# Kernel tuning notes

Hardware: AMD Instinct MI355X
Metric: run time of the kernel (lower is better)

The kernel has to match this reference:

```python
import jax, jax.numpy as jnp
import numpy as np

EPS = 1e-6

def hardswish(x):
    return x * jnp.clip(x + 3.0, 0.0, 6.0) * (1.0 / 6.0)

def setup_inputs() -> dict:
    key = jax.random.key(0)
    ks = jax.random.split(key, 12)
    B, C, T, V, K, O = 64, 64, 512, 25, 3, 64
    x = jax.random.normal(ks[0], (B, C, T, V), jnp.float32)
    A_fixed = jax.random.uniform(ks[1], (K, V, V), jnp.float32)          # fixed structural partitions (buffer)
    A_learned = jax.random.normal(ks[2], (K, V, V), jnp.float32) * 0.01  # learned adjacency (init ~0)
    W_gcn = jax.random.normal(ks[3], (K, O, C), jnp.float32) * (1.0 / np.sqrt(C))  # 1x1 convs, no bias
    gcn_scale = jax.random.uniform(ks[4], (O,), jnp.float32, 0.5, 1.5)   # folded eval-mode BN
    gcn_bias = jax.random.normal(ks[5], (O,), jnp.float32) * 0.05
    tcn_dw = jax.random.normal(ks[6], (O, 1, 9, 1), jnp.float32) * 0.1   # depthwise temporal conv k=9
    tcn_pw = jax.random.normal(ks[7], (O, O), jnp.float32) * (1.0 / np.sqrt(O))  # pointwise conv
    tcn_scale1 = jax.random.uniform(ks[8], (O,), jnp.float32, 0.5, 1.5)
    tcn_bias1 = jax.random.normal(ks[9], (O,), jnp.float32) * 0.05
    tcn_scale2 = jax.random.uniform(ks[10], (O,), jnp.float32, 0.5, 1.5)
    tcn_bias2 = jax.random.normal(ks[11], (O,), jnp.float32) * 0.05
    return {"x": x, "A_fixed": A_fixed, "A_learned": A_learned, "W_gcn": W_gcn,
            "gcn_scale": gcn_scale, "gcn_bias": gcn_bias, "tcn_dw": tcn_dw, "tcn_pw": tcn_pw,
            "tcn_scale1": tcn_scale1, "tcn_bias1": tcn_bias1, "tcn_scale2": tcn_scale2, "tcn_bias2": tcn_bias2}

def _bn(x, scale, bias):
    # eval-mode BatchNorm2d folded to per-channel affine, channel axis=1
    return x * scale[None, :, None, None] + bias[None, :, None, None]

def reference(x, A_fixed, A_learned, W_gcn, gcn_scale, gcn_bias,
              tcn_dw, tcn_pw, tcn_scale1, tcn_bias1, tcn_scale2, tcn_bias2):
    res = x
    K = A_fixed.shape[0]
    # --- EfficientGCN-exact K-way learned-adjacency normalization ---
    A = jnp.abs(A_fixed + A_learned)                       # (K,V,V)
    d = jax.lax.rsqrt(jnp.clip(jnp.sum(A, axis=2), EPS, None))  # torch sum(dim=1) -> row sums, D^{-1/2}
    A_norm = d[:, :, None] * A * d[:, None, :]             # (K,V,V)
    # --- fused adjacency matmul + 1x1 conv accumulate over K ---
    # x:(B,C,T,V) @ A_norm:(K,V,W) then channel mix W_gcn:(K,O,C), averaged over K
    y = jnp.einsum('bctv,kvw,koc->botw', x, A_norm, W_gcn) / K
    y = hardswish(_bn(y, gcn_scale, gcn_bias))
    # --- DepthwiseSepTCN: depthwise temporal conv(k=9,pad=4) -> BN -> hswish -> pointwise -> BN ---
    t = jax.lax.conv_general_dilated(y, tcn_dw, (1, 1), ((4, 4), (0, 0)),
                                     dimension_numbers=('NCHW', 'OIHW', 'NCHW'),
                                     feature_group_count=y.shape[1])
    t = hardswish(_bn(t, tcn_scale1, tcn_bias1))
    t = jnp.einsum('bctv,oc->botv', t, tcn_pw)
    t = _bn(t, tcn_scale2, tcn_bias2)
    # residual is Identity (in_ch==out_ch, stride==1); DropPath rate 0 -> identity
    return hardswish(t + res)
```

## Files before the change

### kernel.cpp

```cpp
#include <hip/hip_runtime.h>
#include <math.h>

typedef unsigned short ushort_t;
typedef __attribute__((ext_vector_type(8))) short short8;
typedef __attribute__((ext_vector_type(4))) short short4v;
typedef __attribute__((ext_vector_type(4))) float f32x4;

#define B_ 64
#define C_ 64
#define T_ 512
#define V_ 25
#define K_ 3
#define O_ 64

__device__ __forceinline__ float hswish(float v) {
    return v * fminf(fmaxf(v + 3.0f, 0.0f), 6.0f) * (1.0f / 6.0f);
}
__device__ __forceinline__ ushort_t f2bf(float f) {
    unsigned u = __float_as_uint(f);
    unsigned r = (u + 0x7FFFu + ((u >> 16) & 1u)) >> 16;
    return (ushort_t)r;
}
__device__ __forceinline__ float bf2f(ushort_t h) {
    return __uint_as_float(((unsigned)h) << 16);
}

__global__ void k0_prep(const float* __restrict__ Af, const float* __restrict__ Al,
                        const float* __restrict__ Wg, const float* __restrict__ pw,
                        ushort_t* __restrict__ An2T, ushort_t* __restrict__ W2,
                        ushort_t* __restrict__ pw2) {
    __shared__ float Aabs[K_ * V_ * V_];
    __shared__ float dsh[K_ * V_];
    int tid = threadIdx.x;
    for (int i = tid; i < K_ * V_ * V_; i += 256) Aabs[i] = fabsf(Af[i] + Al[i]);
    __syncthreads();
    for (int r = tid; r < K_ * V_; r += 256) {
        float s = 0.0f;
        for (int j = 0; j < V_; j++) s += Aabs[r * V_ + j];
        dsh[r] = rsqrtf(fmaxf(s, 1e-6f));
    }
    __syncthreads();
    for (int i = tid; i < 80 * 32; i += 256) {
        int kw = i >> 5, v = i & 31;
        float val = 0.0f;
        if (kw < 75 && v < 25) {
            int k = (kw >= 50) ? 2 : (kw >= 25 ? 1 : 0);
            int w = kw - k * 25;
            val = dsh[k * 25 + v] * Aabs[(k * 25 + v) * 25 + w] * dsh[k * 25 + w];
        }
        An2T[i] = f2bf(val);
    }
    for (int i = tid; i < 64 * 192; i += 256) {
        int o = i / 192, kc = i % 192;
        int k = kc >> 6, c = kc & 63;
        W2[i] = f2bf(Wg[(k * 64 + o) * 64 + c] * (1.0f / 3.0f));
    }
    for (int i = tid; i < 64 * 64; i += 256) pw2[i] = f2bf(pw[i]);
}

__global__ __launch_bounds__(256) void k1_gcn(
    const float* __restrict__ x, const ushort_t* __restrict__ An2T,
    const ushort_t* __restrict__ W2, const float* __restrict__ gs,
    const float* __restrict__ gb, ushort_t* __restrict__ y) {
    __shared__ ushort_t xa2[100 * 200];
    float* xs = (float*)xa2;

    int bid = blockIdx.x;
    int b = bid >> 7;
    int t0 = (bid & 127) * 4;
    int tid = threadIdx.x;
    int wave = tid >> 6, lane = tid & 63;
    int m16 = lane & 15, g = lane >> 4;

#pragma unroll
    for (int i = 0; i < 7; i++) {
        int li = tid + 256 * i;
        if (li < 1600) {
            int c = li / 25, f4 = li % 25;
            const float* src = x + ((size_t)(b * 64 + c) * 512 + t0) * 25 + f4 * 4;
            *(f32x4*)(xs + c * 100 + f4 * 4) = *(const f32x4*)src;
        }
    }

    short8 bfA[5];
#pragma unroll
    for (int n = 0; n < 5; n++)
        bfA[n] = *(const short8*)(An2T + (n * 16 + m16) * 32 + g * 8);

    __syncthreads();

    int v0 = g * 8;
    short8 af[4];
#pragma unroll
    for (int mt = 0; mt < 4; mt++) {
        int ct = (wave * 4 + mt) * 16 + m16;
#pragma unroll
        for (int j = 0; j < 8; j++) {
            int v = v0 + j;
            float f = (v < 25) ? xs[25 * ct + v] : 0.0f;
            af[mt][j] = (short)f2bf(f);
        }
    }
    __syncthreads();

#pragma unroll
    for (int mt = 0; mt < 4; mt++) {
        int Mt = wave * 4 + mt;
        f32x4 acc[5];
#pragma unroll
        for (int n = 0; n < 5; n++) {
            acc[n] = (f32x4){0.f, 0.f, 0.f, 0.f};
            acc[n] = __builtin_amdgcn_mfma_f32_16x16x32_bf16(af[mt], bfA[n], acc[n], 0, 0, 0);
        }
        int cc = Mt * 4 + g;
#pragma unroll
        for (int n = 0; n < 5; n++) {
            int kw = n * 16 + m16;
            if (kw < 75) {
                int k = (kw >= 50) ? 2 : (kw >= 25 ? 1 : 0);
                int w = kw - k * 25;
#pragma unroll
                for (int r = 0; r < 4; r++)
                    xa2[(r * 25 + w) * 200 + k * 64 + cc] = f2bf(acc[n][r]);
            }
        }
    }
    __syncthreads();

    short8 afW[6];
#pragma unroll
    for (int kt = 0; kt < 6; kt++)
        afW[kt] = *(const short8*)(W2 + (wave * 16 + m16) * 192 + kt * 32 + g * 8);
    f32x4 gs4 = *(const f32x4*)(gs + wave * 16 + g * 4);
    f32x4 gb4 = *(const f32x4*)(gb + wave * 16 + g * 4);
    for (int nt = 0; nt < 7; nt++) {
        int tw = nt * 16 + m16;
        int twr = (tw < 100) ? tw : 99;
        f32x4 acc = (f32x4){0.f, 0.f, 0.f, 0.f};
#pragma unroll
        for (int kt = 0; kt < 6; kt++) {
            short8 bf = *(const short8*)(xa2 + twr * 200 + kt * 32 + g * 8);
            acc = __builtin_amdgcn_mfma_f32_16x16x32_bf16(afW[kt], bf, acc, 0, 0, 0);
        }
        if (tw < 100) {
            short4v pack;
#pragma unroll
            for (int r = 0; r < 4; r++) {
                float z = acc[r] * gs4[r] + gb4[r];
                pack[r] = (short)f2bf(hswish(z));
            }
            *(short4v*)(y + ((size_t)b * 12800 + t0 * 25 + tw) * 64 + wave * 16 + g * 4) = pack;
        }
    }
}

__global__ __launch_bounds__(256, 3) void k2_tcn(
    const ushort_t* __restrict__ y, const float* __restrict__ x,
    const float* __restrict__ dw, const ushort_t* __restrict__ pw2,
    const float* __restrict__ s1v, const float* __restrict__ b1v,
    const float* __restrict__ s2v, const float* __restrict__ b2v,
    float* __restrict__ out) {
    __shared__ f32x4 smemv[3264];
    ushort_t* ys = (ushort_t*)smemv;
    float* fb = (float*)smemv;

    int bid = blockIdx.x;
    int b = bid >> 6;
    int t0 = (bid & 63) * 8;
    int tid = threadIdx.x;
    int wave = tid >> 6, lane = tid & 63;
    int m16 = lane & 15, g = lane >> 4;

    const ushort_t* yb = y + (size_t)b * 12800 * 64;
    int tvbase = t0 * 25 - 100;
#pragma unroll
    for (int i = 0; i < 13; i++) {
        int li = tid + 256 * i;
        if (li < 3200) {
            int row = li >> 3;
            int col = (li & 7) * 8;
            int tvg = tvbase + row;
            short8 val = (short8){0, 0, 0, 0, 0, 0, 0, 0};
            if (tvg >= 0 && tvg < 12800)
                val = *(const short8*)(yb + (size_t)tvg * 64 + col);
            *(short8*)(ys + row * 64 + col) = val;
        }
    }
    __syncthreads();

    int cg = tid & 15, c0 = cg * 4;
    float dwc[4][9], s1r[4], b1r[4];
#pragma unroll
    for (int cj = 0; cj < 4; cj++) {
#pragma unroll
        for (int dt = 0; dt < 9; dt++) dwc[cj][dt] = dw[(c0 + cj) * 9 + dt];
        s1r[cj] = s1v[c0 + cj];
        b1r[cj] = b1v[c0 + cj];
    }
    short4v thv[13];
#pragma unroll
    for (int i = 0; i < 13; i++) {
        int tv = (tid >> 4) + 16 * i;
        float a0 = 0, a1 = 0, a2 = 0, a3 = 0;
        if (tv < 200) {
#pragma unroll
            for (int dt = 0; dt < 9; dt++) {
                short4v yv = *(const short4v*)(ys + (tv + dt * 25) * 64 + c0);
                a0 += dwc[0][dt] * bf2f((ushort_t)yv[0]);
                a1 += dwc[1][dt] * bf2f((ushort_t)yv[1]);
                a2 += dwc[2][dt] * bf2f((ushort_t)yv[2]);
                a3 += dwc[3][dt] * bf2f((ushort_t)yv[3]);
            }
        }
        short4v p;
        p[0] = (short)f2bf(hswish(a0 * s1r[0] + b1r[0]));
        p[1] = (short)f2bf(hswish(a1 * s1r[1] + b1r[1]));
        p[2] = (short)f2bf(hswish(a2 * s1r[2] + b1r[2]));
        p[3] = (short)f2bf(hswish(a3 * s1r[3] + b1r[3]));
        thv[i] = p;
    }
    __syncthreads();

#pragma unroll
    for (int i = 0; i < 13; i++) {
        int tv = (tid >> 4) + 16 * i;
        if (tv < 200) *(short4v*)(ys + tv * 64 + c0) = thv[i];
    }
    __syncthreads();

    short8 afP[2];
#pragma unroll
    for (int kt = 0; kt < 2; kt++)
        afP[kt] = *(const short8*)(pw2 + (wave * 16 + m16) * 64 + kt * 32 + g * 8);
    f32x4 s2_4 = *(const f32x4*)(s2v + wave * 16 + g * 4);
    f32x4 b2_4 = *(const f32x4*)(b2v + wave * 16 + g * 4);
    f32x4 accs[13];
#pragma unroll
    for (int nt = 0; nt < 13; nt++) {
        int tw = nt * 16 + m16;
        int twc = (tw < 200) ? tw : 199;
        f32x4 acc = (f32x4){0.f, 0.f, 0.f, 0.f};
#pragma unroll
        for (int kt = 0; kt < 2; kt++) {
            short8 bf = *(const short8*)(ys + twc * 64 + kt * 32 + g * 8);
            acc = __builtin_amdgcn_mfma_f32_16x16x32_bf16(afP[kt], bf, acc, 0, 0, 0);
        }
        accs[nt] = acc;
    }
    __syncthreads();

#pragma unroll
    for (int nt = 0; nt < 13; nt++) {
        int tw = nt * 16 + m16;
        if (tw < 200) {
#pragma unroll
            for (int r = 0; r < 4; r++)
                fb[(wave * 16 + g * 4 + r) * 204 + tw] = accs[nt][r] * s2_4[r] + b2_4[r];
        }
    }
    __syncthreads();

#pragma unroll
    for (int i = 0; i < 13; i++) {
        int l = tid + 256 * i;
        if (l < 3200) {
            int o = l / 50, c4 = l % 50;
            f32x4 v = *(const f32x4*)(fb + o * 204 + c4 * 4);
            size_t gi = (size_t)(b * 64 + o) * 12800 + t0 * 25 + c4 * 4;
            f32x4 xr = *(const f32x4*)(x + gi);
            f32x4 res;
#pragma unroll
            for (int r = 0; r < 4; r++) res[r] = hswish(v[r] + xr[r]);
            *(f32x4*)(out + gi) = res;
        }
    }
}

extern "C" void kernel_launch(void* const* d_in, const int* in_sizes, int n_in,
                              void* d_out, int out_size, void* d_ws, size_t ws_size,
                              hipStream_t stream) {
    const float* x   = (const float*)d_in[0];
    const float* Af  = (const float*)d_in[1];
    const float* Al  = (const float*)d_in[2];
    const float* Wg  = (const float*)d_in[3];
    const float* gs  = (const float*)d_in[4];
    const float* gb  = (const float*)d_in[5];
    const float* dw  = (const float*)d_in[6];
    const float* pw  = (const float*)d_in[7];
    const float* s1v = (const float*)d_in[8];
    const float* b1v = (const float*)d_in[9];
    const float* s2v = (const float*)d_in[10];
    const float* b2v = (const float*)d_in[11];
    float* out = (float*)d_out;

    ushort_t* An2T = (ushort_t*)d_ws;
    ushort_t* W2   = An2T + 2560;
    ushort_t* pw2  = W2 + 12288;
    ushort_t* ybf  = (ushort_t*)((char*)d_ws + 65536);

    k0_prep<<<1, 256, 0, stream>>>(Af, Al, Wg, pw, An2T, W2, pw2);
    k1_gcn<<<B_ * (T_ / 4), 256, 0, stream>>>(x, An2T, W2, gs, gb, ybf);
    k2_tcn<<<B_ * (T_ / 8), 256, 0, stream>>>(ybf, x, dw, pw2, s1v, b1v, s2v, b2v, out);
}
```

Before: 708.5 us.

## Use direct global-to-LDS loads and write TCN output straight from MFMA accumulators

In both kernels the input staging into shared memory now uses global_load_lds 16-byte transfers, so data goes straight into LDS instead of through registers. The k2 interior tiles take this path, while the two boundary time tiles keep the zero-padded register copy. The k2 epilogue no longer stages results through a shared-memory transpose. Each lane fuses BN2, the residual add and hardswish and writes scalar floats directly from the accumulators. This removes two barriers and an LDS round trip, at the cost of narrower, less coalesced residual reads and output stores.

```diff
diff --git a/kernel.cpp b/kernel.cpp
--- a/kernel.cpp
+++ b/kernel.cpp
@@ -78,7 +78,10 @@
         if (li < 1600) {
             int c = li / 25, f4 = li % 25;
             const float* src = x + ((size_t)(b * 64 + c) * 512 + t0) * 25 + f4 * 4;
-            *(f32x4*)(xs + c * 100 + f4 * 4) = *(const f32x4*)src;
+            __builtin_amdgcn_global_load_lds(
+                (const __attribute__((address_space(1))) unsigned*)src,
+                (__attribute__((address_space(3))) unsigned*)(xs + li * 4),
+                16, 0, 0);
         }
     }
 
@@ -160,9 +163,7 @@
     const float* __restrict__ s1v, const float* __restrict__ b1v,
     const float* __restrict__ s2v, const float* __restrict__ b2v,
     float* __restrict__ out) {
-    __shared__ f32x4 smemv[3264];
-    ushort_t* ys = (ushort_t*)smemv;
-    float* fb = (float*)smemv;
+    __shared__ ushort_t ys[400 * 64];
 
     int bid = blockIdx.x;
     int b = bid >> 6;
@@ -173,17 +174,31 @@
 
     const ushort_t* yb = y + (size_t)b * 12800 * 64;
     int tvbase = t0 * 25 - 100;
-#pragma unroll
-    for (int i = 0; i < 13; i++) {
-        int li = tid + 256 * i;
-        if (li < 3200) {
-            int row = li >> 3;
-            int col = (li & 7) * 8;
-            int tvg = tvbase + row;
-            short8 val = (short8){0, 0, 0, 0, 0, 0, 0, 0};
-            if (tvg >= 0 && tvg < 12800)
-                val = *(const short8*)(yb + (size_t)tvg * 64 + col);
-            *(short8*)(ys + row * 64 + col) = val;
+    if (t0 != 0 && t0 != 504) {
+        const ushort_t* src0 = yb + (size_t)tvbase * 64;
+#pragma unroll
+        for (int i = 0; i < 13; i++) {
+            int li = tid + 256 * i;
+            if (li < 3200) {
+                __builtin_amdgcn_global_load_lds(
+                    (const __attribute__((address_space(1))) unsigned*)(src0 + li * 8),
+                    (__attribute__((address_space(3))) unsigned*)(ys + li * 8),
+                    16, 0, 0);
+            }
+        }
+    } else {
+#pragma unroll
+        for (int i = 0; i < 13; i++) {
+            int li = tid + 256 * i;
+            if (li < 3200) {
+                int row = li >> 3;
+                int col = (li & 7) * 8;
+                int tvg = tvbase + row;
+                short8 val = (short8){0, 0, 0, 0, 0, 0, 0, 0};
+                if (tvg >= 0 && tvg < 12800)
+                    val = *(const short8*)(yb + (size_t)tvg * 64 + col);
+                *(short8*)(ys + row * 64 + col) = val;
+            }
         }
     }
     __syncthreads();
@@ -234,8 +249,6 @@
         afP[kt] = *(const short8*)(pw2 + (wave * 16 + m16) * 64 + kt * 32 + g * 8);
     f32x4 s2_4 = *(const f32x4*)(s2v + wave * 16 + g * 4);
     f32x4 b2_4 = *(const f32x4*)(b2v + wave * 16 + g * 4);
-    f32x4 accs[13];
-#pragma unroll
     for (int nt = 0; nt < 13; nt++) {
         int tw = nt * 16 + m16;
         int twc = (tw < 200) ? tw : 199;
@@ -245,33 +258,14 @@
             short8 bf = *(const short8*)(ys + twc * 64 + kt * 32 + g * 8);
             acc = __builtin_amdgcn_mfma_f32_16x16x32_bf16(afP[kt], bf, acc, 0, 0, 0);
         }
-        accs[nt] = acc;
-    }
-    __syncthreads();
-
-#pragma unroll
-    for (int nt = 0; nt < 13; nt++) {
-        int tw = nt * 16 + m16;
         if (tw < 200) {
 #pragma unroll
-            for (int r = 0; r < 4; r++)
-                fb[(wave * 16 + g * 4 + r) * 204 + tw] = accs[nt][r] * s2_4[r] + b2_4[r];
-        }
-    }
-    __syncthreads();
-
-#pragma unroll
-    for (int i = 0; i < 13; i++) {
-        int l = tid + 256 * i;
-        if (l < 3200) {
-            int o = l / 50, c4 = l % 50;
-            f32x4 v = *(const f32x4*)(fb + o * 204 + c4 * 4);
-            size_t gi = (size_t)(b * 64 + o) * 12800 + t0 * 25 + c4 * 4;
-            f32x4 xr = *(const f32x4*)(x + gi);
-            f32x4 res;
-#pragma unroll
-            for (int r = 0; r < 4; r++) res[r] = hswish(v[r] + xr[r]);
-            *(f32x4*)(out + gi) = res;
+            for (int r = 0; r < 4; r++) {
+                int o = wave * 16 + g * 4 + r;
+                size_t idx = (size_t)(b * 64 + o) * 12800 + t0 * 25 + tw;
+                float z = acc[r] * s2_4[r] + b2_4[r] + x[idx];
+                out[idx] = hswish(z);
+            }
         }
     }
 }
```

New measurement: 644.9 us. -9.0%, faster.
